# Performance work log

Hardware: AMD Instinct MI355X
Metric: run time of the kernel (lower is better)

Reference implementation:

```python
import jax, jax.numpy as jnp
import numpy as np

B, IN, OUT = 256, 1024, 1024


def choquet_cardinal(z):
    """Discrete Choquet integral over last axis with cardinality measure mu(A)=|A|/n.
    ChI(x) = sum_i (x_(i) - x_(i-1)) * mu(A_i), x_(0)=0, mu(A_i)=(n-i+1)/n.
    """
    n = z.shape[-1]
    xs = jnp.sort(z, axis=-1)  # ascending
    # diffs[..., 0] = x_(1); diffs[..., i] = x_(i+1) - x_(i)
    diffs = jnp.concatenate([xs[..., :1], jnp.diff(xs, axis=-1)], axis=-1)
    mu = (n - jnp.arange(n, dtype=xs.dtype)) / n  # 1, (n-1)/n, ..., 1/n
    return jnp.einsum('...i,i->...', diffs, mu)


def setup_inputs() -> dict:
    key = jax.random.key(0)
    kx, kw, kb = jax.random.split(key, 3)
    x = jax.random.normal(kx, (B, 1, IN), dtype=jnp.float32)
    weight = jax.random.normal(kw, (IN, OUT), dtype=jnp.float32) * 0.02
    bias = jax.random.normal(kb, (IN, OUT), dtype=jnp.float32) * 0.02
    return {"x": x, "weight": weight, "bias": bias}


def reference(x, weight, bias):
    # z: [B, OUT, IN] = x * W^T + b^T (elementwise with broadcast)
    z = x * weight.T + bias.T
    chi = choquet_cardinal(z)  # [B, OUT]
    return jax.nn.sigmoid(chi)
```

## Files before the change

### kernel.cpp

```cpp
#include <hip/hip_runtime.h>
#include <math.h>


#define BATCH   256
#define IN_DIM  1024
#define OUT_DIM 1024

#define APACK_OFF 0
#define WPACK_OFF (512 * 1024)

#define NWTASK_A   512
#define NWTASK_W  4096
#define NBLK_PREP ((NWTASK_A + NWTASK_W) / 4)

typedef __bf16 bf16x8 __attribute__((ext_vector_type(8)));
typedef float  f32x4  __attribute__((ext_vector_type(4)));

__global__ __launch_bounds__(256) void chad_prep(
    const float* __restrict__ x,
    const float* __restrict__ w,
    const float* __restrict__ bias,
    unsigned char* __restrict__ ws)
{
    __bf16* apack = (__bf16*)(ws + APACK_OFF);
    __bf16* wpack = (__bf16*)(ws + WPACK_OFF);

    const int t    = threadIdx.x;
    const int lane = t & 63;
    const int wv   = t >> 6;
    const int g    = blockIdx.x * 4 + wv;
    const int l16  = lane & 15;
    const int quad = lane >> 4;

    if (g < NWTASK_A) {
        const int mt = g >> 5, s = g & 31;
        const float* src = x + (size_t)(mt * 16 + l16) * IN_DIM + s * 32 + quad * 8;
        const float4 v0 = *(const float4*)src;
        const float4 v1 = *(const float4*)(src + 4);
        bf16x8 o;
        o[0] = (__bf16)v0.x; o[1] = (__bf16)v0.y; o[2] = (__bf16)v0.z; o[3] = (__bf16)v0.w;
        o[4] = (__bf16)v1.x; o[5] = (__bf16)v1.y; o[6] = (__bf16)v1.z; o[7] = (__bf16)v1.w;
        *(bf16x8*)(apack + (size_t)g * 512 + lane * 8) = o;
    } else {
        const int wt = g - NWTASK_A;
        const int nt = wt >> 6, s = wt & 63;
        const float* base = (s < 32) ? w : bias;
        const int k = (s & 31) * 32;
        const float* src = base + (size_t)(k + quad * 8) * OUT_DIM + nt * 16 + l16;
        bf16x8 o;
        #pragma unroll
        for (int j = 0; j < 8; ++j) o[j] = (__bf16)src[(size_t)j * OUT_DIM];
        *(bf16x8*)(wpack + (size_t)wt * 512 + lane * 8) = o;
    }
}

__global__ __launch_bounds__(256) void chad_gemm(
    const unsigned char* __restrict__ ws,
    float* __restrict__ out)
{
    const __bf16* apack = (const __bf16*)(ws + APACK_OFF);
    const __bf16* wpack = (const __bf16*)(ws + WPACK_OFF);

    __shared__ float red[4][64][4];

    const int t    = threadIdx.x;
    const int lane = t & 63;
    const int wv   = t >> 6;
    const int mt   = blockIdx.x >> 6;
    const int nt   = blockIdx.x & 63;

    const __bf16* ab  = apack + ((size_t)(mt * 32 + wv * 8) * 64 + lane) * 8;
    const __bf16* wb  = wpack + ((size_t)(nt * 64 + wv * 8) * 64 + lane) * 8;
    const __bf16* wb2 = wpack + ((size_t)(nt * 64 + 32 + wv * 8) * 64 + lane) * 8;

    bf16x8 af[8], bw[8], bb[8];
    #pragma unroll
    for (int i = 0; i < 8; ++i) {
        af[i] = *(const bf16x8*)(ab  + (size_t)i * 512);
        bw[i] = *(const bf16x8*)(wb  + (size_t)i * 512);
        bb[i] = *(const bf16x8*)(wb2 + (size_t)i * 512);
    }

    bf16x8 one8;
    #pragma unroll
    for (int j = 0; j < 8; ++j) one8[j] = (__bf16)1.0f;

    f32x4 acc = {0.f, 0.f, 0.f, 0.f};
    #pragma unroll
    for (int i = 0; i < 8; ++i)
        acc = __builtin_amdgcn_mfma_f32_16x16x32_bf16(af[i], bw[i], acc, 0, 0, 0);
    #pragma unroll
    for (int i = 0; i < 8; ++i)
        acc = __builtin_amdgcn_mfma_f32_16x16x32_bf16(one8, bb[i], acc, 0, 0, 0);

    *(f32x4*)&red[wv][lane][0] = acc;
    __syncthreads();

    const int row = t >> 4, col = t & 15;
    const int rl  = ((row >> 2) << 4) + col;
    const int rr  = row & 3;
    float v = red[0][rl][rr] + red[1][rl][rr] + red[2][rl][rr] + red[3][rl][rr];
    v *= (1.0f / (float)IN_DIM);
    out[(size_t)(mt * 16 + row) * OUT_DIM + nt * 16 + col] = 1.0f / (1.0f + __expf(-v));
}

extern "C" void kernel_launch(void* const* d_in, const int* in_sizes, int n_in,
                              void* d_out, int out_size, void* d_ws, size_t ws_size,
                              hipStream_t stream) {
    const float* x  = (const float*)d_in[0];
    const float* w  = (const float*)d_in[1];
    const float* b  = (const float*)d_in[2];
    float* out = (float*)d_out;

    chad_prep<<<NBLK_PREP, 256, 0, stream>>>(x, w, b, (unsigned char*)d_ws);
    chad_gemm<<<(BATCH / 16) * (OUT_DIM / 16), 256, 0, stream>>>(
        (const unsigned char*)d_ws, out);
}
```

Measured before the change: 70.62 us.

## Enlarge GEMM output tile to 32x32 to reuse A/W fragments and bias sums

Each block of the GEMM now computes a 32x32 output tile instead of 16x16. Each A fragment is reused against two W column tiles, and each W fragment against two A row tiles. The bias column-sum MFMA is computed once per column tile rather than once per row tile. This cuts global fragment loads and redundant bias MFMAs, but it quarters the grid to 256 blocks, which raises per-thread register and LDS use and lowers parallelism.

```diff
diff --git a/kernel.cpp b/kernel.cpp
--- a/kernel.cpp
+++ b/kernel.cpp
@@ -54,54 +54,86 @@
     }
 }
 
-__global__ __launch_bounds__(256) void chad_gemm(
+__global__ __launch_bounds__(256, 1) void chad_gemm(
     const unsigned char* __restrict__ ws,
     float* __restrict__ out)
 {
     const __bf16* apack = (const __bf16*)(ws + APACK_OFF);
     const __bf16* wpack = (const __bf16*)(ws + WPACK_OFF);
 
-    __shared__ float red[4][64][4];
+    __shared__ float red[4][6][64][4];
 
     const int t    = threadIdx.x;
     const int lane = t & 63;
     const int wv   = t >> 6;
-    const int mt   = blockIdx.x >> 6;
-    const int nt   = blockIdx.x & 63;
+    const int mt   = blockIdx.x >> 5;
+    const int nt   = blockIdx.x & 31;
 
-    const __bf16* ab  = apack + ((size_t)(mt * 32 + wv * 8) * 64 + lane) * 8;
-    const __bf16* wb  = wpack + ((size_t)(nt * 64 + wv * 8) * 64 + lane) * 8;
-    const __bf16* wb2 = wpack + ((size_t)(nt * 64 + 32 + wv * 8) * 64 + lane) * 8;
-
-    bf16x8 af[8], bw[8], bb[8];
+    const __bf16* ab = apack + ((size_t)((mt * 2) * 32 + wv * 8) * 64 + lane) * 8;
+    bf16x8 af[2][8];
     #pragma unroll
-    for (int i = 0; i < 8; ++i) {
-        af[i] = *(const bf16x8*)(ab  + (size_t)i * 512);
-        bw[i] = *(const bf16x8*)(wb  + (size_t)i * 512);
-        bb[i] = *(const bf16x8*)(wb2 + (size_t)i * 512);
-    }
+    for (int r = 0; r < 2; ++r)
+        #pragma unroll
+        for (int i = 0; i < 8; ++i)
+            af[r][i] = *(const bf16x8*)(ab + ((size_t)r * 32 + i) * 512);
 
     bf16x8 one8;
     #pragma unroll
     for (int j = 0; j < 8; ++j) one8[j] = (__bf16)1.0f;
 
-    f32x4 acc = {0.f, 0.f, 0.f, 0.f};
+    f32x4 accw[2][2] = {{{0.f,0.f,0.f,0.f},{0.f,0.f,0.f,0.f}},
+                        {{0.f,0.f,0.f,0.f},{0.f,0.f,0.f,0.f}}};
+    f32x4 accb[2]    = {{0.f,0.f,0.f,0.f},{0.f,0.f,0.f,0.f}};
+
     #pragma unroll
-    for (int i = 0; i < 8; ++i)
-        acc = __builtin_amdgcn_mfma_f32_16x16x32_bf16(af[i], bw[i], acc, 0, 0, 0);
+    for (int c = 0; c < 2; ++c) {
+        const __bf16* wb = wpack + ((size_t)((nt * 2 + c) * 64 + wv * 8) * 64 + lane) * 8;
+        bf16x8 wf[8], bf8[8];
+        #pragma unroll
+        for (int i = 0; i < 8; ++i) wf[i]  = *(const bf16x8*)(wb + (size_t)i * 512);
+        #pragma unroll
+        for (int i = 0; i < 8; ++i) bf8[i] = *(const bf16x8*)(wb + (size_t)(32 + i) * 512);
+        #pragma unroll
+        for (int i = 0; i < 8; ++i) {
+            accw[0][c] = __builtin_amdgcn_mfma_f32_16x16x32_bf16(af[0][i], wf[i], accw[0][c], 0, 0, 0);
+            accw[1][c] = __builtin_amdgcn_mfma_f32_16x16x32_bf16(af[1][i], wf[i], accw[1][c], 0, 0, 0);
+            accb[c]    = __builtin_amdgcn_mfma_f32_16x16x32_bf16(one8,     bf8[i], accb[c],   0, 0, 0);
+        }
+    }
+
     #pragma unroll
-    for (int i = 0; i < 8; ++i)
-        acc = __builtin_amdgcn_mfma_f32_16x16x32_bf16(one8, bb[i], acc, 0, 0, 0);
-
-    *(f32x4*)&red[wv][lane][0] = acc;
+    for (int r = 0; r < 2; ++r)
+        #pragma unroll
+        for (int c = 0; c < 2; ++c)
+            *(f32x4*)&red[wv][r * 2 + c][lane][0] = accw[r][c];
+    #pragma unroll
+    for (int c = 0; c < 2; ++c)
+        *(f32x4*)&red[wv][4 + c][lane][0] = accb[c];
     __syncthreads();
 
-    const int row = t >> 4, col = t & 15;
-    const int rl  = ((row >> 2) << 4) + col;
-    const int rr  = row & 3;
-    float v = red[0][rl][rr] + red[1][rl][rr] + red[2][rl][rr] + red[3][rl][rr];
-    v *= (1.0f / (float)IN_DIM);
-    out[(size_t)(mt * 16 + row) * OUT_DIM + nt * 16 + col] = 1.0f / (1.0f + __expf(-v));
+    const int row  = t >> 3;
+    const int cb   = (t & 7) * 4;
+    const int r    = row >> 4;
+    const int row16 = row & 15;
+    const int rr   = row16 & 3;
+    const int rlh  = (row16 >> 2) << 4;
+    const float inv_n = 1.0f / (float)IN_DIM;
+
+    float4 o;
+    #pragma unroll
+    for (int j = 0; j < 4; ++j) {
+        const int col   = cb + j;
+        const int c     = col >> 4;
+        const int col16 = col & 15;
+        const int a     = r * 2 + c;
+        float v  = red[0][a][rlh + col16][rr] + red[1][a][rlh + col16][rr]
+                 + red[2][a][rlh + col16][rr] + red[3][a][rlh + col16][rr];
+        float cs = red[0][4 + c][col16][0] + red[1][4 + c][col16][0]
+                 + red[2][4 + c][col16][0] + red[3][4 + c][col16][0];
+        const float z = (v + cs) * inv_n;
+        (&o.x)[j] = 1.0f / (1.0f + __expf(-z));
+    }
+    *(float4*)&out[(size_t)(mt * 32 + row) * OUT_DIM + nt * 32 + cb] = o;
 }
 
 extern "C" void kernel_launch(void* const* d_in, const int* in_sizes, int n_in,
@@ -113,6 +145,6 @@
     float* out = (float*)d_out;
 
     chad_prep<<<NBLK_PREP, 256, 0, stream>>>(x, w, b, (unsigned char*)d_ws);
-    chad_gemm<<<(BATCH / 16) * (OUT_DIM / 16), 256, 0, stream>>>(
+    chad_gemm<<<(BATCH / 32) * (OUT_DIM / 32), 256, 0, stream>>>(
         (const unsigned char*)d_ws, out);
 }
```

New measurement: 71.34 us. About the same (+1.0%).
